# Kernel optimization log

Measured on AMD Instinct MI355X. Metric: run time of the kernel, lower is better.

## Reference

```python
import jax, jax.numpy as jnp
import numpy as np

V, MAXLEN, D, FF, H, L = 50257, 1024, 768, 3072, 12, 12
HD = D // H


def _ln(x, w, b, eps=1e-5):
    mu = jnp.mean(x, axis=-1, keepdims=True)
    var = jnp.var(x, axis=-1, keepdims=True)
    return (x - mu) * jax.lax.rsqrt(var + eps) * w + b


def setup_inputs() -> dict:
    key = jax.random.key(0)
    ks = jax.random.split(key, 16)
    s = 0.02
    inp = {
        "tokens": jax.random.randint(ks[0], (2, 1024), 0, V),
        "tok_embed": jax.random.normal(ks[1], (V, D), jnp.float32) * s,
        "pos_embed": jax.random.normal(ks[2], (MAXLEN, D), jnp.float32) * s,
        # stacked per-layer params, weights stored [in, out]
        "qkv_w": jax.random.normal(ks[3], (L, D, 3 * D), jnp.float32) * s,
        "qkv_b": jnp.zeros((L, 3 * D), jnp.float32),
        "proj_w": jax.random.normal(ks[4], (L, D, D), jnp.float32) * s,
        "proj_b": jnp.zeros((L, D), jnp.float32),
        "ln1_w": jnp.ones((L, D), jnp.float32),
        "ln1_b": jnp.zeros((L, D), jnp.float32),
        "ln2_w": jnp.ones((L, D), jnp.float32),
        "ln2_b": jnp.zeros((L, D), jnp.float32),
        "fc1_w": jax.random.normal(ks[5], (L, D, FF), jnp.float32) * s,
        "fc1_b": jnp.zeros((L, FF), jnp.float32),
        "fc2_w": jax.random.normal(ks[6], (L, FF, D), jnp.float32) * s,
        "fc2_b": jnp.zeros((L, D), jnp.float32),
        "lnf_w": jnp.ones((D,), jnp.float32),
        "lnf_b": jnp.zeros((D,), jnp.float32),
    }
    return inp


def _gpt2(tokens, tok_embed, pos_embed, qkv_w, qkv_b, proj_w, proj_b,
          ln1_w, ln1_b, ln2_w, ln2_b, fc1_w, fc1_b, fc2_w, fc2_b, lnf_w, lnf_b):
    B, T = tokens.shape
    x = tok_embed[tokens] + pos_embed[jnp.arange(T)][None, :, :]  # [B,T,D]
    causal = jnp.tril(jnp.ones((T, T), bool))[None, None]          # [1,1,T,T]
    neg = jnp.finfo(x.dtype).min

    def block(x, p):
        (qw, qb, pw, pb, l1w, l1b, l2w, l2b, f1w, f1b, f2w, f2b) = p
        h = _ln(x, l1w, l1b)
        qkv = h @ qw + qb                                          # [B,T,3D]
        q, k, v = jnp.split(qkv, 3, axis=-1)
        q = q.reshape(B, T, H, HD).transpose(0, 2, 1, 3)           # [B,H,T,HD]
        k = k.reshape(B, T, H, HD).transpose(0, 2, 1, 3)
        v = v.reshape(B, T, H, HD).transpose(0, 2, 1, 3)
        att = jnp.einsum('bhqd,bhkd->bhqk', q, k) / np.sqrt(HD).astype(x.dtype)
        att = jnp.where(causal, att, neg)
        att = jax.nn.softmax(att, axis=-1)
        o = jnp.einsum('bhqk,bhkd->bhqd', att, v)
        o = o.transpose(0, 2, 1, 3).reshape(B, T, D)
        x = x + o @ pw + pb
        h2 = _ln(x, l2w, l2b)
        ff = jax.nn.gelu(h2 @ f1w + f1b, approximate=True) @ f2w + f2b
        return x + ff, None

    params = (qkv_w, qkv_b, proj_w, proj_b, ln1_w, ln1_b, ln2_w, ln2_b,
              fc1_w, fc1_b, fc2_w, fc2_b)
    x, _ = jax.lax.scan(block, x, params)
    x = _ln(x, lnf_w, lnf_b)
    return x @ tok_embed.T                                         # tied lm_head [B,T,V]


def reference(tokens, tok_embed, pos_embed, qkv_w, qkv_b, proj_w, proj_b,
              ln1_w, ln1_b, ln2_w, ln2_b, fc1_w, fc1_b, fc2_w, fc2_b,
              lnf_w, lnf_b):
    return _gpt2(tokens, tok_embed, pos_embed, qkv_w, qkv_b, proj_w, proj_b,
                 ln1_w, ln1_b, ln2_w, ln2_b, fc1_w, fc1_b, fc2_w, fc2_b,
                 lnf_w, lnf_b)
```

## Files before the change

kernel.cpp:

```cpp
#include <hip/hip_runtime.h>

#define TT 1024
#define DD 768
#define FFD 3072
#define NH 12
#define NL 12
#define HDIM 64
#define VOC 50257
#define BT 2048

typedef __attribute__((ext_vector_type(8))) __bf16 bf16x8;
typedef __attribute__((ext_vector_type(4))) float f32x4;
typedef __attribute__((ext_vector_type(4))) unsigned short u16x4;
typedef unsigned short u16;

static __device__ __forceinline__ u16 f2bf(float f) {
  unsigned int u = __float_as_uint(f);
  u += 0x7FFF + ((u >> 16) & 1);
  return (u16)(u >> 16);
}

static __device__ __forceinline__ void load_lds16(const u16* g, u16* l) {
  __builtin_amdgcn_global_load_lds(
      (const __attribute__((address_space(1))) unsigned int*)g,
      (__attribute__((address_space(3))) unsigned int*)l, 16, 0, 0);
}

__global__ __launch_bounds__(256) void transpose_convert(
    const float* __restrict__ in, u16* __restrict__ out, int R, int C) {
  __shared__ float tile[32][33];
  const long long zo = (long long)blockIdx.z * R * C;
  const int c0 = blockIdx.x * 32, r0 = blockIdx.y * 32;
  const int tx = threadIdx.x & 31, ty = threadIdx.x >> 5;
#pragma unroll
  for (int i = 0; i < 32; i += 8)
    tile[ty + i][tx] = in[zo + (long long)(r0 + ty + i) * C + c0 + tx];
  __syncthreads();
#pragma unroll
  for (int i = 0; i < 32; i += 8)
    out[zo + (long long)(c0 + ty + i) * R + r0 + tx] = f2bf(tile[tx][ty + i]);
}

__global__ void convert_bf16(const float* __restrict__ in, u16* __restrict__ out,
                             long long n) {
  long long i = (long long)blockIdx.x * 256 + threadIdx.x;
  const long long stride = (long long)gridDim.x * 256;
  for (; i < n; i += stride) out[i] = f2bf(in[i]);
}

__global__ __launch_bounds__(256) void embed_kernel(
    const int* __restrict__ tokens, const float* __restrict__ tokE,
    const float* __restrict__ posE, float* __restrict__ x) {
  const int row = blockIdx.x;
  const int t = row & (TT - 1);
  const int tok = tokens[row];
  const int tid = threadIdx.x;
#pragma unroll
  for (int c = 0; c < 3; ++c) {
    int d = tid + c * 256;
    x[(long long)row * DD + d] = tokE[(long long)tok * DD + d] + posE[(long long)t * DD + d];
  }
}

__global__ __launch_bounds__(256) void layernorm_bf16(
    const float* __restrict__ x, const float* __restrict__ w,
    const float* __restrict__ b, u16* __restrict__ out) {
  const int row = blockIdx.x;
  const float* xr = x + (long long)row * DD;
  const int tid = threadIdx.x;
  float v[3];
  float s = 0.f, s2 = 0.f;
#pragma unroll
  for (int c = 0; c < 3; ++c) {
    float t = xr[tid + c * 256];
    v[c] = t; s += t; s2 += t * t;
  }
  for (int off = 32; off; off >>= 1) {
    s += __shfl_down(s, off, 64);
    s2 += __shfl_down(s2, off, 64);
  }
  __shared__ float rs[8];
  if ((tid & 63) == 0) { rs[tid >> 6] = s; rs[4 + (tid >> 6)] = s2; }
  __syncthreads();
  s = rs[0] + rs[1] + rs[2] + rs[3];
  s2 = rs[4] + rs[5] + rs[6] + rs[7];
  const float mu = s * (1.0f / DD);
  const float var = s2 * (1.0f / DD) - mu * mu;
  const float inv = rsqrtf(var + 1e-5f);
  u16* o = out + (long long)row * DD;
#pragma unroll
  for (int c = 0; c < 3; ++c) {
    int d = tid + c * 256;
    o[d] = f2bf((v[c] - mu) * inv * w[d] + b[d]);
  }
}

__global__ __launch_bounds__(256, 3) void flash_attn(
    const u16* __restrict__ qkv, const u16* __restrict__ vT,
    u16* __restrict__ attn) {
  __shared__ __align__(16) u16 Qs[64 * 64];
  __shared__ __align__(16) u16 Ks0[64 * 64];
  __shared__ __align__(16) u16 Ks1[64 * 64];
  __shared__ __align__(16) u16 Vs0[64 * 64];
  __shared__ __align__(16) u16 Vs1[64 * 64];
  __shared__ __align__(16) u16 Ps[4 * 16 * 72];

  const int id = blockIdx.x;
  const int qt = 15 - id / 24;
  const int z = id % 24;
  const int b = z / NH, h = z - (z / NH) * NH;
  const int q0 = qt * 64;

  const int tid = threadIdx.x;
  const int lane = tid & 63;
  const int wave = __builtin_amdgcn_readfirstlane(tid >> 6);
  const int mf = lane & 15;
  const int quad = lane >> 4;

  const int srow = wave * 16 + (lane >> 3);
  const int srow1 = srow + 8;
  const int sch0 = (((lane & 7) ^ ((srow >> 1) & 7))) * 8;
  const int sch1 = (((lane & 7) ^ ((srow1 >> 1) & 7))) * 8;
  const int lb = wave * 1024;

  const u16* qk_base = qkv + (long long)b * TT * 2304 + h * 64;

  auto stageKV = [&](u16* Kd, u16* Vd, int kv0) {
    load_lds16(qk_base + (long long)(kv0 + srow) * 2304 + 768 + sch0, Kd + lb);
    load_lds16(qk_base + (long long)(kv0 + srow1) * 2304 + 768 + sch1, Kd + lb + 512);
    load_lds16(vT + (long long)(z * 64 + srow) * 1024 + kv0 + sch0, Vd + lb);
    load_lds16(vT + (long long)(z * 64 + srow1) * 1024 + kv0 + sch1, Vd + lb + 512);
  };

  load_lds16(qk_base + (long long)(q0 + srow) * 2304 + sch0, Qs + lb);
  load_lds16(qk_base + (long long)(q0 + srow1) * 2304 + sch1, Qs + lb + 512);
  stageKV(Ks0, Vs0, 0);
  __syncthreads();

  bf16x8 qfr[2];
  {
    const int r = wave * 16 + mf;
    const int sw = (r >> 1) & 7;
#pragma unroll
    for (int ks = 0; ks < 2; ++ks)
      qfr[ks] = *(const bf16x8*)(Qs + r * 64 + (((ks * 4 + quad) ^ sw) * 8));
  }

  f32x4 oacc[4] = {};
  float mrun = -1e30f, lrun = 0.f;
  u16 *Kc = Ks0, *Vc = Vs0, *Kn = Ks1, *Vn = Vs1;

  for (int t = 0; t <= qt; ++t) {
    if (t < qt) stageKV(Kn, Vn, (t + 1) * 64);
    const int diag = (t == qt);

    f32x4 sacc[4] = {};
#pragma unroll
    for (int ks = 0; ks < 2; ++ks)
#pragma unroll
      for (int i = 0; i < 4; ++i) {
        const int r = i * 16 + mf;
        bf16x8 kfr = *(const bf16x8*)(Kc + r * 64 + (((ks * 4 + quad) ^ ((r >> 1) & 7)) * 8));
        sacc[i] = __builtin_amdgcn_mfma_f32_16x16x32_bf16(kfr, qfr[ks], sacc[i], 0, 0, 0);
      }

    float pv[4][4];
    float tmax = -1e30f;
#pragma unroll
    for (int i = 0; i < 4; ++i)
#pragma unroll
      for (int r = 0; r < 4; ++r) {
        float v = sacc[i][r] * 0.125f;
        if (diag) {
          const int kvl = i * 16 + quad * 4 + r;
          if (kvl > wave * 16 + mf) v = -1e30f;
        }
        pv[i][r] = v;
        tmax = fmaxf(tmax, v);
      }
    tmax = fmaxf(tmax, __shfl_xor(tmax, 16, 64));
    tmax = fmaxf(tmax, __shfl_xor(tmax, 32, 64));
    const float mnew = fmaxf(mrun, tmax);
    const float fac = __expf(mrun - mnew);
    float lsum = 0.f;
#pragma unroll
    for (int i = 0; i < 4; ++i)
#pragma unroll
      for (int r = 0; r < 4; ++r) {
        float e = __expf(pv[i][r] - mnew);
        pv[i][r] = e;
        lsum += e;
      }
    lsum += __shfl_xor(lsum, 16, 64);
    lsum += __shfl_xor(lsum, 32, 64);
    lrun = lrun * fac + lsum;
    mrun = mnew;

    float fo[4];
#pragma unroll
    for (int r = 0; r < 4; ++r) fo[r] = __shfl(fac, (lane & 48) | (quad * 4 + r), 64);
#pragma unroll
    for (int j = 0; j < 4; ++j)
#pragma unroll
      for (int r = 0; r < 4; ++r) oacc[j][r] *= fo[r];

#pragma unroll
    for (int i = 0; i < 4; ++i) {
      u16x4 pk;
#pragma unroll
      for (int r = 0; r < 4; ++r) pk[r] = f2bf(pv[i][r]);
      *(u16x4*)(Ps + wave * 1152 + mf * 72 + i * 16 + quad * 4) = pk;
    }
#pragma unroll
    for (int ks = 0; ks < 2; ++ks) {
      bf16x8 pfr = *(const bf16x8*)(Ps + wave * 1152 + mf * 72 + ks * 32 + quad * 8);
#pragma unroll
      for (int j = 0; j < 4; ++j) {
        const int r = j * 16 + mf;
        bf16x8 vfr = *(const bf16x8*)(Vc + r * 64 + (((ks * 4 + quad) ^ ((r >> 1) & 7)) * 8));
        oacc[j] = __builtin_amdgcn_mfma_f32_16x16x32_bf16(pfr, vfr, oacc[j], 0, 0, 0);
      }
    }
    __syncthreads();
    u16* tk = Kc; Kc = Kn; Kn = tk;
    u16* tv = Vc; Vc = Vn; Vn = tv;
  }

  const float linv = 1.0f / lrun;
  float li[4];
#pragma unroll
  for (int r = 0; r < 4; ++r) li[r] = __shfl(linv, (lane & 48) | (quad * 4 + r), 64);
#pragma unroll
  for (int j = 0; j < 4; ++j)
#pragma unroll
    for (int r = 0; r < 4; ++r) {
      const int q = q0 + wave * 16 + quad * 4 + r;
      const int d = j * 16 + mf;
      attn[(long long)(b * TT + q) * 768 + h * 64 + d] = f2bf(oacc[j][r] * li[r]);
    }
}

enum { EPI_F32 = 0, EPI_BF16_BIAS = 1, EPI_BF16_BIAS_GELU = 2, EPI_F32_BIAS_RES = 3,
       EPI_BF16 = 4, EPI_QKV = 5 };

template <int EPI>
__global__ __launch_bounds__(256, 3) void gemm_nt(
    const u16* __restrict__ A, const u16* __restrict__ Bm,
    const float* __restrict__ bias, const float* __restrict__ resid,
    void* __restrict__ Cout, u16* __restrict__ vtAux,
    int M, int N, int K, int lda, int ldb, int ldc,
    long long aHi, long long aLo, long long bHi, long long bLo,
    long long cHi, long long cLo, int Hdiv, int swapxy,
    int xcdChunk) {
  __shared__ __align__(16) u16 As0[128 * 32];
  __shared__ __align__(16) u16 As1[128 * 32];
  __shared__ __align__(16) u16 Bs0[128 * 32];
  __shared__ __align__(16) u16 Bs1[128 * 32];
  const int z = blockIdx.z;
  const int zb = z / Hdiv, zh = z - zb * Hdiv;
  const u16* Ab = A + zb * aHi + zh * aLo;
  const u16* Bb = Bm + zb * bHi + zh * bLo;
  const long long cOff = (long long)zb * cHi + (long long)zh * cLo;

  int rx = blockIdx.x, ry = blockIdx.y;
  if (xcdChunk) {
    const int id = ry * gridDim.x + rx;
    const int w = (id & 7) * xcdChunk + (id >> 3);
    rx = w % gridDim.x;
    ry = w / gridDim.x;
  }
  const int bx = swapxy ? ry : rx;
  const int by = swapxy ? rx : ry;
  const int m0 = by * 128;
  const int n0 = bx * 128;

  const int tid = threadIdx.x;
  const int lane = tid & 63;
  const int wave = __builtin_amdgcn_readfirstlane(tid >> 6);
  const int wm = (wave >> 1) * 64;
  const int wn = (wave & 1) * 64;
  const int mf = lane & 15;
  const int quad = lane >> 4;

  const int sr0 = wave * 32 + (lane >> 2);
  const int sr1 = sr0 + 16;
  const int sc0 = ((lane & 3) ^ ((sr0 >> 1) & 3)) * 8;
  const int sc1 = ((lane & 3) ^ ((sr1 >> 1) & 3)) * 8;
  int br0 = n0 + sr0; if (br0 >= N) br0 = N - 1;
  int br1 = n0 + sr1; if (br1 >= N) br1 = N - 1;
  const u16* agp0 = Ab + (long long)(m0 + sr0) * lda + sc0;
  const u16* agp1 = Ab + (long long)(m0 + sr1) * lda + sc1;
  const u16* bgp0 = Bb + (long long)br0 * ldb + sc0;
  const u16* bgp1 = Bb + (long long)br1 * ldb + sc1;
  const int woff = wave * 1024;

  auto stage = [&](u16* Ad, u16* Bd, int kk) {
    load_lds16(agp0 + kk, Ad + woff);
    load_lds16(agp1 + kk, Ad + woff + 512);
    load_lds16(bgp0 + kk, Bd + woff);
    load_lds16(bgp1 + kk, Bd + woff + 512);
  };

  int aoff[4], boff[4];
#pragma unroll
  for (int i = 0; i < 4; ++i) {
    const int ar = wm + i * 16 + mf;
    aoff[i] = ar * 32 + ((quad ^ ((ar >> 1) & 3)) * 8);
    const int br = wn + i * 16 + mf;
    boff[i] = br * 32 + ((quad ^ ((br >> 1) & 3)) * 8);
  }

  f32x4 acc[4][4] = {};

  auto compute = [&](const u16* Asb, const u16* Bsb) {
    bf16x8 afr[4], bfr[4];
#pragma unroll
    for (int i = 0; i < 4; ++i) afr[i] = *(const bf16x8*)(Asb + aoff[i]);
#pragma unroll
    for (int j = 0; j < 4; ++j) bfr[j] = *(const bf16x8*)(Bsb + boff[j]);
#pragma unroll
    for (int i = 0; i < 4; ++i)
#pragma unroll
      for (int j = 0; j < 4; ++j)
        acc[i][j] = __builtin_amdgcn_mfma_f32_16x16x32_bf16(afr[i], bfr[j], acc[i][j], 0, 0, 0);
  };

  stage(As0, Bs0, 0);
  __syncthreads();
  for (int k0 = 0; k0 < K; k0 += 64) {
    if (k0 + 32 < K) stage(As1, Bs1, k0 + 32);
    compute(As0, Bs0);
    __syncthreads();
    if (k0 + 64 < K) stage(As0, Bs0, k0 + 64);
    compute(As1, Bs1);
    __syncthreads();
  }

#pragma unroll
  for (int j = 0; j < 4; ++j) {
    const int col = n0 + wn + j * 16 + mf;
    if (col >= N) continue;
    const float bv = (EPI == EPI_BF16_BIAS || EPI == EPI_BF16_BIAS_GELU ||
                      EPI == EPI_F32_BIAS_RES || EPI == EPI_QKV)
                         ? bias[col] : 0.0f;
    if (EPI == EPI_QKV && col >= 1536) {
      const int hd = col - 1536;
#pragma unroll
      for (int i = 0; i < 4; ++i) {
        const int t0 = m0 + wm + i * 16 + quad * 4;
        u16x4 pk;
#pragma unroll
        for (int r = 0; r < 4; ++r) pk[r] = f2bf(acc[i][j][r] + bv);
        const int b_ = t0 >> 10;
        const long long vi =
            ((long long)((b_ * NH + (hd >> 6)) * 64 + (hd & 63))) * 1024 + (t0 & 1023);
        *(u16x4*)(vtAux + vi) = pk;
      }
      continue;
    }
#pragma unroll
    for (int i = 0; i < 4; ++i) {
#pragma unroll
      for (int r = 0; r < 4; ++r) {
        const int row = m0 + wm + i * 16 + quad * 4 + r;
        float v = acc[i][j][r] + bv;
        if (EPI == EPI_BF16_BIAS_GELU) {
          float u = v + 0.044715f * v * v * v;
          v = 0.5f * v * (1.0f + tanhf(0.7978845608028654f * u));
        }
        const long long ci = cOff + (long long)row * ldc + col;
        if (EPI == EPI_F32_BIAS_RES) {
          ((float*)Cout)[ci] = resid[(long long)row * ldc + col] + v;
        } else if (EPI == EPI_F32) {
          ((float*)Cout)[ci] = v;
        } else {
          ((u16*)Cout)[ci] = f2bf(v);
        }
      }
    }
  }
}

extern "C" void kernel_launch(void* const* d_in, const int* in_sizes, int n_in,
                              void* d_out, int out_size, void* d_ws, size_t ws_size,
                              hipStream_t stream) {
  const int* tokens      = (const int*)d_in[0];
  const float* tok_embed = (const float*)d_in[1];
  const float* pos_embed = (const float*)d_in[2];
  const float* qkv_w     = (const float*)d_in[3];
  const float* qkv_b     = (const float*)d_in[4];
  const float* proj_w    = (const float*)d_in[5];
  const float* proj_b    = (const float*)d_in[6];
  const float* ln1_w     = (const float*)d_in[7];
  const float* ln1_b     = (const float*)d_in[8];
  const float* ln2_w     = (const float*)d_in[9];
  const float* ln2_b     = (const float*)d_in[10];
  const float* fc1_w     = (const float*)d_in[11];
  const float* fc1_b     = (const float*)d_in[12];
  const float* fc2_w     = (const float*)d_in[13];
  const float* fc2_b     = (const float*)d_in[14];
  const float* lnf_w     = (const float*)d_in[15];
  const float* lnf_b     = (const float*)d_in[16];

  if (ws_size < 440u * 1024u * 1024u) return;

  char* p = (char*)d_ws;
  auto alloc = [&](size_t bytes) {
    void* r = (void*)p;
    p += (bytes + 255) & ~(size_t)255;
    return r;
  };
  u16* wq   = (u16*)alloc((size_t)NL * 2304 * 768 * 2);
  u16* wp   = (u16*)alloc((size_t)NL * 768 * 768 * 2);
  u16* w1   = (u16*)alloc((size_t)NL * 3072 * 768 * 2);
  u16* w2   = (u16*)alloc((size_t)NL * 768 * 3072 * 2);
  u16* te   = (u16*)alloc((size_t)VOC * 768 * 2);
  float* x  = (float*)alloc((size_t)BT * 768 * 4);
  u16* hbuf = (u16*)alloc((size_t)BT * 768 * 2);
  u16* qkv  = (u16*)alloc((size_t)BT * 2304 * 2);
  u16* vT   = (u16*)alloc((size_t)24 * 64 * 1024 * 2);
  u16* attn = (u16*)alloc((size_t)BT * 768 * 2);
  u16* ff   = (u16*)alloc((size_t)BT * 3072 * 2);
  u16* xf   = (u16*)alloc((size_t)BT * 768 * 2);

  transpose_convert<<<dim3(2304 / 32, 768 / 32, NL), 256, 0, stream>>>(qkv_w, wq, 768, 2304);
  transpose_convert<<<dim3(768 / 32, 768 / 32, NL), 256, 0, stream>>>(proj_w, wp, 768, 768);
  transpose_convert<<<dim3(3072 / 32, 768 / 32, NL), 256, 0, stream>>>(fc1_w, w1, 768, 3072);
  transpose_convert<<<dim3(768 / 32, 3072 / 32, NL), 256, 0, stream>>>(fc2_w, w2, 3072, 768);
  convert_bf16<<<4096, 256, 0, stream>>>(tok_embed, te, (long long)VOC * 768);
  embed_kernel<<<BT, 256, 0, stream>>>(tokens, tok_embed, pos_embed, x);

  for (int l = 0; l < NL; ++l) {
    layernorm_bf16<<<BT, 256, 0, stream>>>(x, ln1_w + l * 768, ln1_b + l * 768, hbuf);
    gemm_nt<EPI_QKV><<<dim3(2304 / 128, BT / 128, 1), 256, 0, stream>>>(
        hbuf, wq + (size_t)l * 2304 * 768, qkv_b + l * 2304, nullptr, qkv, vT,
        BT, 2304, 768, 768, 768, 2304, 0, 0, 0, 0, 0, 0, 1, 0, 288 / 8);
    flash_attn<<<384, 256, 0, stream>>>(qkv, vT, attn);
    gemm_nt<EPI_F32_BIAS_RES><<<dim3(768 / 128, BT / 128, 1), 256, 0, stream>>>(
        attn, wp + (size_t)l * 768 * 768, proj_b + l * 768, x, x, nullptr,
        BT, 768, 768, 768, 768, 768, 0, 0, 0, 0, 0, 0, 1, 0, 96 / 8);
    layernorm_bf16<<<BT, 256, 0, stream>>>(x, ln2_w + l * 768, ln2_b + l * 768, hbuf);
    gemm_nt<EPI_BF16_BIAS_GELU><<<dim3(3072 / 128, BT / 128, 1), 256, 0, stream>>>(
        hbuf, w1 + (size_t)l * 3072 * 768, fc1_b + l * 3072, nullptr, ff, nullptr,
        BT, 3072, 768, 768, 768, 3072, 0, 0, 0, 0, 0, 0, 1, 0, 384 / 8);
    gemm_nt<EPI_F32_BIAS_RES><<<dim3(768 / 128, BT / 128, 1), 256, 0, stream>>>(
        ff, w2 + (size_t)l * 768 * 3072, fc2_b + l * 768, x, x, nullptr,
        BT, 768, 3072, 3072, 3072, 768, 0, 0, 0, 0, 0, 0, 1, 0, 96 / 8);
  }
  layernorm_bf16<<<BT, 256, 0, stream>>>(x, lnf_w, lnf_b, xf);
  gemm_nt<EPI_F32><<<dim3(BT / 128, (VOC + 127) / 128, 1), 256, 0, stream>>>(
      xf, te, nullptr, nullptr, (float*)d_out, nullptr,
      BT, VOC, 768, 768, 768, VOC, 0, 0, 0, 0, 0, 0, 1, 1, 6288 / 8);
}
```

Before: 2.813 ms.

## Split-K the proj and fc2 GEMMs with atomic accumulation into the residual

```diff
diff --git a/kernel.cpp b/kernel.cpp
--- a/kernel.cpp
+++ b/kernel.cpp
@@ -241,7 +241,7 @@
 }
 
 enum { EPI_F32 = 0, EPI_BF16_BIAS = 1, EPI_BF16_BIAS_GELU = 2, EPI_F32_BIAS_RES = 3,
-       EPI_BF16 = 4, EPI_QKV = 5 };
+       EPI_BF16 = 4, EPI_QKV = 5, EPI_SPLITK_RES = 6 };
 
 template <int EPI>
 __global__ __launch_bounds__(256, 3) void gemm_nt(
@@ -251,15 +251,23 @@
     int M, int N, int K, int lda, int ldb, int ldc,
     long long aHi, long long aLo, long long bHi, long long bLo,
     long long cHi, long long cLo, int Hdiv, int swapxy,
-    int xcdChunk) {
+    int xcdChunk, int kSplit) {
   __shared__ __align__(16) u16 As0[128 * 32];
   __shared__ __align__(16) u16 As1[128 * 32];
   __shared__ __align__(16) u16 Bs0[128 * 32];
   __shared__ __align__(16) u16 Bs1[128 * 32];
   const int z = blockIdx.z;
-  const int zb = z / Hdiv, zh = z - zb * Hdiv;
-  const u16* Ab = A + zb * aHi + zh * aLo;
-  const u16* Bb = Bm + zb * bHi + zh * bLo;
+  int zb = 0, zh = 0;
+  long long koff = 0;
+  if (kSplit > 1) {
+    const int slice = K / kSplit;
+    koff = (long long)z * slice;
+    K = slice;
+  } else {
+    zb = z / Hdiv; zh = z - zb * Hdiv;
+  }
+  const u16* Ab = A + zb * aHi + zh * aLo + koff;
+  const u16* Bb = Bm + zb * bHi + zh * bLo + koff;
   const long long cOff = (long long)zb * cHi + (long long)zh * cLo;
 
   int rx = blockIdx.x, ry = blockIdx.y;
@@ -340,9 +348,11 @@
   for (int j = 0; j < 4; ++j) {
     const int col = n0 + wn + j * 16 + mf;
     if (col >= N) continue;
-    const float bv = (EPI == EPI_BF16_BIAS || EPI == EPI_BF16_BIAS_GELU ||
-                      EPI == EPI_F32_BIAS_RES || EPI == EPI_QKV)
-                         ? bias[col] : 0.0f;
+    float bv = 0.0f;
+    if (EPI == EPI_BF16_BIAS || EPI == EPI_BF16_BIAS_GELU || EPI == EPI_F32_BIAS_RES ||
+        EPI == EPI_QKV)
+      bv = bias[col];
+    if (EPI == EPI_SPLITK_RES && z == 0) bv = bias[col];
     if (EPI == EPI_QKV && col >= 1536) {
       const int hd = col - 1536;
 #pragma unroll
@@ -369,7 +379,9 @@
           v = 0.5f * v * (1.0f + tanhf(0.7978845608028654f * u));
         }
         const long long ci = cOff + (long long)row * ldc + col;
-        if (EPI == EPI_F32_BIAS_RES) {
+        if (EPI == EPI_SPLITK_RES) {
+          atomicAdd((float*)Cout + ci, v);
+        } else if (EPI == EPI_F32_BIAS_RES) {
           ((float*)Cout)[ci] = resid[(long long)row * ldc + col] + v;
         } else if (EPI == EPI_F32) {
           ((float*)Cout)[ci] = v;
@@ -434,21 +446,21 @@
     layernorm_bf16<<<BT, 256, 0, stream>>>(x, ln1_w + l * 768, ln1_b + l * 768, hbuf);
     gemm_nt<EPI_QKV><<<dim3(2304 / 128, BT / 128, 1), 256, 0, stream>>>(
         hbuf, wq + (size_t)l * 2304 * 768, qkv_b + l * 2304, nullptr, qkv, vT,
-        BT, 2304, 768, 768, 768, 2304, 0, 0, 0, 0, 0, 0, 1, 0, 288 / 8);
+        BT, 2304, 768, 768, 768, 2304, 0, 0, 0, 0, 0, 0, 1, 0, 288 / 8, 1);
     flash_attn<<<384, 256, 0, stream>>>(qkv, vT, attn);
-    gemm_nt<EPI_F32_BIAS_RES><<<dim3(768 / 128, BT / 128, 1), 256, 0, stream>>>(
-        attn, wp + (size_t)l * 768 * 768, proj_b + l * 768, x, x, nullptr,
-        BT, 768, 768, 768, 768, 768, 0, 0, 0, 0, 0, 0, 1, 0, 96 / 8);
+    gemm_nt<EPI_SPLITK_RES><<<dim3(768 / 128, BT / 128, 2), 256, 0, stream>>>(
+        attn, wp + (size_t)l * 768 * 768, proj_b + l * 768, nullptr, x, nullptr,
+        BT, 768, 768, 768, 768, 768, 0, 0, 0, 0, 0, 0, 1, 0, 96 / 8, 2);
     layernorm_bf16<<<BT, 256, 0, stream>>>(x, ln2_w + l * 768, ln2_b + l * 768, hbuf);
     gemm_nt<EPI_BF16_BIAS_GELU><<<dim3(3072 / 128, BT / 128, 1), 256, 0, stream>>>(
         hbuf, w1 + (size_t)l * 3072 * 768, fc1_b + l * 3072, nullptr, ff, nullptr,
-        BT, 3072, 768, 768, 768, 3072, 0, 0, 0, 0, 0, 0, 1, 0, 384 / 8);
-    gemm_nt<EPI_F32_BIAS_RES><<<dim3(768 / 128, BT / 128, 1), 256, 0, stream>>>(
-        ff, w2 + (size_t)l * 768 * 3072, fc2_b + l * 768, x, x, nullptr,
-        BT, 768, 3072, 3072, 3072, 768, 0, 0, 0, 0, 0, 0, 1, 0, 96 / 8);
+        BT, 3072, 768, 768, 768, 3072, 0, 0, 0, 0, 0, 0, 1, 0, 384 / 8, 1);
+    gemm_nt<EPI_SPLITK_RES><<<dim3(768 / 128, BT / 128, 4), 256, 0, stream>>>(
+        ff, w2 + (size_t)l * 768 * 3072, fc2_b + l * 768, nullptr, x, nullptr,
+        BT, 768, 3072, 3072, 3072, 768, 0, 0, 0, 0, 0, 0, 1, 0, 96 / 8, 4);
   }
   layernorm_bf16<<<BT, 256, 0, stream>>>(x, lnf_w, lnf_b, xf);
   gemm_nt<EPI_F32><<<dim3(BT / 128, (VOC + 127) / 128, 1), 256, 0, stream>>>(
       xf, te, nullptr, nullptr, (float*)d_out, nullptr,
-      BT, VOC, 768, 768, 768, VOC, 0, 0, 0, 0, 0, 0, 1, 1, 6288 / 8);
-}
+      BT, VOC, 768, 768, 768, VOC, 0, 0, 0, 0, 0, 0, 1, 1, 6288 / 8, 1);
+}
```

Result: faster. 2.580 ms (-8.3%).
